# Kernel optimization log

Measured on AMD Instinct MI355X. Metric: run time of the kernel, lower is better.

Reference implementation:

```python
import jax, jax.numpy as jnp
import numpy as np

N, L, V, D, E, NL = 50000, 32, 5000, 128, 800000, 3
P, B = 5000, 64

def setup_inputs() -> dict:
    key = jax.random.key(0)
    ks = jax.random.split(key, 6)
    x = jax.random.randint(ks[0], (N, L), 0, V)            # token ids, 0 = pad
    edge_index = jax.random.randint(ks[1], (2, E), 0, N)   # [2,E] src,dst
    pool_idx = jnp.arange(N) // (N // P)                   # node -> pooled supernode
    node_batch = pool_idx * B // P                         # node -> graph id (grouped, as in torch loop)
    embed = jax.random.normal(ks[2], (V, D), jnp.float32) * 0.02
    W_l = jax.random.normal(ks[3], (NL, D, D), jnp.float32) / np.sqrt(D)
    W_r = jax.random.normal(ks[4], (NL, D, D), jnp.float32) / np.sqrt(D)
    b = jnp.zeros((NL, D), jnp.float32)
    return dict(x=x, edge_index=edge_index, pool_idx=pool_idx, node_batch=node_batch,
                num_pooled=P, embed=embed, W_l=W_l, W_r=W_r, b=b)

def reference(x, edge_index, pool_idx, node_batch, num_pooled, embed, W_l, W_r, b):
    n = x.shape[0]
    dt = embed.dtype
    # masked mean-pool of token embeddings (pad id = 0), length clamped to >=1
    mask = (x != 0)
    lengths = jnp.clip(mask.sum(axis=1), 1, None).astype(dt)          # [N]
    h = (embed[x] * mask[..., None].astype(dt)).sum(axis=1) / lengths[:, None]  # [N,D]
    src, dst = edge_index[0], edge_index[1]
    deg = jnp.clip(jax.ops.segment_sum(jnp.ones(src.shape[0], dt), dst, num_segments=n), 1.0, None)
    # SAGEConv layers: mean-aggregate neighbors, lin_l(agg)+bias + lin_r(self), relu
    # (dropout p=0.5 is identity in eval mode)
    for i in range(W_l.shape[0]):
        agg = jax.ops.segment_sum(h[src], dst, num_segments=n) / deg[:, None]
        h = jax.nn.relu(agg @ W_l[i] + b[i] + h @ W_r[i])
    # global mean pool over supernodes
    cnt = jnp.clip(jax.ops.segment_sum(jnp.ones(n, dt), pool_idx, num_segments=num_pooled), 1.0, None)
    x_pooled = jax.ops.segment_sum(h, pool_idx, num_segments=num_pooled) / cnt[:, None]
    # global max pool of graph ids -> pooled batch vector
    batch_pooled = jax.ops.segment_max(node_batch, pool_idx, num_segments=num_pooled)
    # coalesced pooled edges without self-loops, as a dense boolean adjacency
    sp, dp = pool_idx[src], pool_idx[dst]
    adj = jnp.zeros((num_pooled, num_pooled), jnp.bool_).at[sp, dp].set(True)
    adj = adj & ~jnp.eye(num_pooled, dtype=jnp.bool_)
    return x_pooled, adj, batch_pooled
```

## Files before the change

### kernel.cpp

```cpp
#include <hip/hip_runtime.h>
#include <limits.h>

#define D 128
#define NBK 768
#define EB  2048

typedef __attribute__((ext_vector_type(8))) short bf16x8;
typedef __attribute__((ext_vector_type(4))) float f32x4;

static __device__ __forceinline__ unsigned short f2bf(float f) {
    unsigned u = __builtin_bit_cast(unsigned, f);
    u += 0x7FFFu + ((u >> 16) & 1u);
    return (unsigned short)(u >> 16);
}
static __device__ __forceinline__ float bf2f(unsigned u16) {
    unsigned u = u16 << 16;
    return __builtin_bit_cast(float, u);
}
static __device__ __forceinline__ bf16x8 load_frag(const unsigned short* p) {
    uint4 v = *(const uint4*)p;
    return __builtin_bit_cast(bf16x8, v);
}
static __device__ __forceinline__ void acc8(float* a, uint4 v) {
    a[0] += bf2f(v.x & 0xffff); a[1] += bf2f(v.x >> 16);
    a[2] += bf2f(v.y & 0xffff); a[3] += bf2f(v.y >> 16);
    a[4] += bf2f(v.z & 0xffff); a[5] += bf2f(v.z >> 16);
    a[6] += bf2f(v.w & 0xffff); a[7] += bf2f(v.w >> 16);
}
static __device__ __forceinline__ ushort4 pack4(const float* a, float s) {
    ushort4 o;
    o.x = f2bf(a[0] * s); o.y = f2bf(a[1] * s);
    o.z = f2bf(a[2] * s); o.w = f2bf(a[3] * s);
    return o;
}

__global__ __launch_bounds__(256) void zero_k(float4* __restrict__ b, size_t nb)
{
    size_t i = (size_t)blockIdx.x * 256 + threadIdx.x;
    if (i < nb) b[i] = make_float4(0.f, 0.f, 0.f, 0.f);
}

__global__ __launch_bounds__(256) void epack_k(
    const float* __restrict__ embed, unsigned short* __restrict__ e16, int n4)
{
    int i = blockIdx.x * 256 + threadIdx.x;
    if (i >= n4) return;
    float4 v = *(const float4*)&embed[(size_t)i * 4];
    ushort4 o;
    o.x = f2bf(v.x); o.y = f2bf(v.y); o.z = f2bf(v.z); o.w = f2bf(v.w);
    *(ushort4*)&e16[(size_t)i * 4] = o;
}

__global__ __launch_bounds__(256) void embed_pool_k(
    const int* __restrict__ x, const unsigned short* __restrict__ e16,
    unsigned short* __restrict__ h16, int n, int L)
{
    __shared__ int toks[16][32];
    int t = threadIdx.x;
    int sub = t >> 4, s = t & 15;
    int node = blockIdx.x * 16 + sub;
    for (int j = t; j < 16 * L; j += 256) {
        int nd = blockIdx.x * 16 + j / L;
        toks[j / L][j % L] = (nd < n) ? x[(size_t)nd * L + (j % L)] : 0;
    }
    __syncthreads();
    if (node >= n) return;
    float acc[8] = {};
    int cnt = 0;
    for (int l = 0; l < L; ++l) {
        int tok = toks[sub][l];
        if (tok != 0) {
            acc8(acc, *(const uint4*)&e16[(size_t)tok * D + s * 8]);
            cnt++;
        }
    }
    float inv = 1.0f / (float)(cnt > 0 ? cnt : 1);
    ushort4 lo = pack4(acc, inv), hi = pack4(acc + 4, inv);
    *(ushort4*)&h16[(size_t)node * D + s * 8]     = lo;
    *(ushort4*)&h16[(size_t)node * D + s * 8 + 4] = hi;
}

__global__ __launch_bounds__(256) void wpack_k(
    const float* __restrict__ Wl, const float* __restrict__ Wr,
    unsigned short* __restrict__ Wp, int NL)
{
    int idx = blockIdx.x * 256 + threadIdx.x;
    if (idx >= NL * 2 * 16384) return;
    int m = idx >> 14;
    int r = idx & 16383;
    int j = r & 7;
    int lane = (r >> 3) & 63;
    int cb = (r >> 9) & 7;
    int kb = (r >> 12) & 3;
    const float* W = ((m & 1) ? Wr : Wl) + (size_t)(m >> 1) * D * D;
    int k = kb * 32 + (lane >> 4) * 8 + j;
    int c = cb * 16 + (lane & 15);
    Wp[idx] = f2bf(W[(size_t)k * D + c]);
}

__global__ __launch_bounds__(256) void deghist_k(
    const int* __restrict__ ei, const int* __restrict__ pool,
    int* __restrict__ degall, int E, int n, int P, int nblk)
{
    __shared__ int hist[NBK];
    int t = threadIdx.x;
    for (int i = t; i < NBK; i += 256) hist[i] = 0;
    __syncthreads();
    int base = blockIdx.x * EB;
    int lim = min(E, base + EB);
    for (int e = base + t; e < lim; e += 256) {
        int src = ei[e], dst = ei[E + e];
        atomicAdd(&degall[dst], 1);
        int sp = pool[src], dp = pool[dst];
        if (sp != dp) atomicAdd(&hist[(sp * P + dp) >> 15], 1);
    }
    __syncthreads();
    for (int i = t; i < NBK; i += 256)
        degall[n + i * nblk + blockIdx.x] = hist[i];
}

__global__ __launch_bounds__(256) void scan_partial_k(
    const int* __restrict__ deg, int* __restrict__ bsum, int n)
{
    int b = blockIdx.x, t = threadIdx.x;
    int i0 = b * 1024 + t * 4;
    int s = 0;
    #pragma unroll
    for (int k = 0; k < 4; ++k) { int i = i0 + k; if (i < n) s += deg[i]; }
    for (int off = 32; off > 0; off >>= 1) s += __shfl_down(s, off, 64);
    __shared__ int sm4[4];
    if ((t & 63) == 0) sm4[t >> 6] = s;
    __syncthreads();
    if (t == 0) bsum[b] = sm4[0] + sm4[1] + sm4[2] + sm4[3];
}

__global__ __launch_bounds__(512) void scan_bsum_k(
    const int* __restrict__ bsum, int* __restrict__ boff, int nb)
{
    __shared__ int sm[512];
    int t = threadIdx.x;
    sm[t] = (t < nb) ? bsum[t] : 0;
    __syncthreads();
    for (int off = 1; off < 512; off <<= 1) {
        int add = (t >= off) ? sm[t - off] : 0;
        __syncthreads();
        sm[t] += add;
        __syncthreads();
    }
    if (t < nb) boff[t] = (t > 0) ? sm[t - 1] : 0;
}

__global__ __launch_bounds__(256) void scan_final_k(
    const int* __restrict__ deg, const int* __restrict__ boff,
    int* __restrict__ rp, int n)
{
    __shared__ int sm[256];
    int b = blockIdx.x, t = threadIdx.x;
    int i0 = b * 1024 + t * 4;
    int v[4];
    #pragma unroll
    for (int k = 0; k < 4; ++k) { int i = i0 + k; v[k] = (i < n) ? deg[i] : 0; }
    v[1] += v[0]; v[2] += v[1]; v[3] += v[2];
    sm[t] = v[3];
    __syncthreads();
    for (int off = 1; off < 256; off <<= 1) {
        int add = (t >= off) ? sm[t - off] : 0;
        __syncthreads();
        sm[t] += add;
        __syncthreads();
    }
    int base = boff[b] + ((t > 0) ? sm[t - 1] : 0);
    if (b == 0 && t == 0) rp[0] = 0;
    #pragma unroll
    for (int k = 0; k < 4; ++k) {
        int i = i0 + k;
        if (i < n) rp[i + 1] = base + v[k];
    }
}

__global__ __launch_bounds__(256) void csr_scatter_k(
    const int* __restrict__ ei, const int* __restrict__ rpall,
    int* __restrict__ cur, int* __restrict__ col, int E)
{
    int e = blockIdx.x * 256 + threadIdx.x;
    if (e >= E) return;
    int src = ei[e], dst = ei[E + e];
    int pos = atomicAdd(&cur[dst], 1);
    col[rpall[dst] + pos] = src;
}

__global__ __launch_bounds__(256) void bkt_scatter_k(
    const int* __restrict__ ei, const int* __restrict__ rpall,
    const int* __restrict__ pool, int* __restrict__ kbuf,
    int E, int n, int P, int nblk)
{
    __shared__ int off[NBK];
    int t = threadIdx.x;
    for (int i = t; i < NBK; i += 256)
        off[i] = rpall[n + i * nblk + blockIdx.x] - E;
    __syncthreads();
    int base = blockIdx.x * EB;
    int lim = min(E, base + EB);
    for (int e = base + t; e < lim; e += 256) {
        int src = ei[e], dst = ei[E + e];
        int sp = pool[src], dp = pool[dst];
        if (sp != dp) {
            int key = sp * P + dp;
            int kpos = atomicAdd(&off[key >> 15], 1);
            kbuf[kpos] = key;
        }
    }
}

__global__ __launch_bounds__(256) void adj_write_k(
    const int* __restrict__ rpall, const int* __restrict__ kbuf,
    float* __restrict__ adj, int E, int n, int nblk, int ns)
{
    int b = blockIdx.x;
    int s = rpall[n + b * nblk] - E;
    int e = (b == NBK - 1) ? (rpall[ns] - E) : (rpall[n + (b + 1) * nblk] - E);
    for (int i = s + threadIdx.x; i < e; i += 256)
        adj[(size_t)kbuf[i]] = 1.0f;
}

__global__ __launch_bounds__(256) void aggregate_k(
    const unsigned short* __restrict__ h16, const int* __restrict__ rp,
    const int* __restrict__ col, unsigned short* __restrict__ agg16, int n)
{
    int node = blockIdx.x * 4 + (threadIdx.x >> 6);
    int lane = threadIdx.x & 63;
    if (node >= n) return;
    int beg = rp[node], end = rp[node + 1];
    int q = lane >> 4, s = lane & 15;
    float acc[8] = {};
    int e = beg + q;
    for (; e + 4 < end; e += 8) {
        int s0 = col[e], s1 = col[e + 4];
        uint4 v0 = *(const uint4*)&h16[(size_t)s0 * D + s * 8];
        uint4 v1 = *(const uint4*)&h16[(size_t)s1 * D + s * 8];
        acc8(acc, v0);
        acc8(acc, v1);
    }
    if (e < end)
        acc8(acc, *(const uint4*)&h16[(size_t)col[e] * D + s * 8]);
    #pragma unroll
    for (int k = 0; k < 8; ++k) {
        acc[k] += __shfl_xor(acc[k], 16, 64);
        acc[k] += __shfl_xor(acc[k], 32, 64);
    }
    if (q == 0) {
        int dg = end - beg;
        float inv = 1.0f / (float)(dg > 0 ? dg : 1);
        ushort4 lo = pack4(acc, inv), hi = pack4(acc + 4, inv);
        *(ushort4*)&agg16[(size_t)node * D + s * 8]     = lo;
        *(ushort4*)&agg16[(size_t)node * D + s * 8 + 4] = hi;
    }
}

__global__ __launch_bounds__(256) void sage_gemm_mfma_k(
    const unsigned short* __restrict__ agg16, unsigned short* __restrict__ h16,
    const unsigned short* __restrict__ Wp,
    const float* __restrict__ bias, int n)
{
    int t = threadIdx.x;
    int w = t >> 6, lane = t & 63;
    int node0 = blockIdx.x * 128 + w * 32;
    int row = lane & 15, g = lane >> 4;

    f32x4 acc[2][8];
    #pragma unroll
    for (int i = 0; i < 2; ++i)
        #pragma unroll
        for (int c = 0; c < 8; ++c)
            acc[i][c] = (f32x4){0.f, 0.f, 0.f, 0.f};

    float bs[8];
    #pragma unroll
    for (int cb = 0; cb < 8; ++cb) bs[cb] = bias[cb * 16 + row];

    bool ok0 = (node0 < n);
    bool ok1 = (node0 + 16 < n);

    #pragma unroll
    for (int kb = 0; kb < 8; ++kb) {
        const unsigned short* Asrc = (kb < 4) ? agg16 : h16;
        int ko = (kb & 3) * 32 + g * 8;
        bf16x8 a0 = (bf16x8){0,0,0,0,0,0,0,0};
        bf16x8 a1 = a0;
        if (ok0) a0 = load_frag(&Asrc[(size_t)(node0 + row) * D + ko]);
        if (ok1) a1 = load_frag(&Asrc[(size_t)(node0 + 16 + row) * D + ko]);
        const unsigned short* wp = Wp + ((kb < 4) ? 0 : 16384) + (size_t)(kb & 3) * 4096;
        #pragma unroll
        for (int cb = 0; cb < 8; ++cb) {
            bf16x8 b = load_frag(&wp[(cb * 64 + lane) * 8]);
            acc[0][cb] = __builtin_amdgcn_mfma_f32_16x16x32_bf16(a0, b, acc[0][cb], 0, 0, 0);
            acc[1][cb] = __builtin_amdgcn_mfma_f32_16x16x32_bf16(a1, b, acc[1][cb], 0, 0, 0);
        }
    }

    #pragma unroll
    for (int rg = 0; rg < 2; ++rg) {
        int nb = node0 + rg * 16;
        if (nb >= n) break;
        #pragma unroll
        for (int cb = 0; cb < 8; ++cb) {
            int c = cb * 16 + row;
            #pragma unroll
            for (int j = 0; j < 4; ++j) {
                int node = nb + g * 4 + j;
                float v = fmaxf(acc[rg][cb][j] + bs[cb], 0.f);
                h16[(size_t)node * D + c] = f2bf(v);
            }
        }
    }
}

__global__ __launch_bounds__(128) void poolmean_k(
    const unsigned short* __restrict__ h16, const int* __restrict__ pool,
    const int* __restrict__ nbatch, float* __restrict__ outx,
    float* __restrict__ outb, int n, int P)
{
    int p = blockIdx.x;
    int d = threadIdx.x;
    int lo = 0, hi = n;
    while (lo < hi) { int mid = (lo + hi) >> 1; if (pool[mid] < p) lo = mid + 1; else hi = mid; }
    int s = lo;
    hi = n;
    while (lo < hi) { int mid = (lo + hi) >> 1; if (pool[mid] < p + 1) lo = mid + 1; else hi = mid; }
    int e = lo;
    float sum = 0.f;
    for (int i = s; i < e; ++i) sum += bf2f(h16[(size_t)i * D + d]);
    int c = e - s;
    outx[(size_t)p * D + d] = sum / (float)(c > 0 ? c : 1);
    if (d == 0) {
        int bm = INT_MIN;
        for (int i = s; i < e; ++i) bm = max(bm, nbatch[i]);
        outb[p] = (float)bm;
    }
}

extern "C" void kernel_launch(void* const* d_in, const int* in_sizes, int n_in,
                              void* d_out, int out_size, void* d_ws, size_t ws_size,
                              hipStream_t stream)
{
    const int*   x      = (const int*)d_in[0];
    const int*   ei     = (const int*)d_in[1];
    const int*   pool   = (const int*)d_in[2];
    const int*   nbatch = (const int*)d_in[3];
    const float* embed  = (const float*)d_in[5];
    const float* Wl     = (const float*)d_in[6];
    const float* Wr     = (const float*)d_in[7];
    const float* bias   = (const float*)d_in[8];

    const int N  = in_sizes[2];
    const int L  = in_sizes[0] / N;
    const int E  = in_sizes[1] / 2;
    const int VD = in_sizes[5];
    const int NL = in_sizes[6] / (D * D);
    const int P  = 5000;

    float* out_x   = (float*)d_out;
    float* out_adj = out_x + (size_t)P * D;
    float* out_b   = out_adj + (size_t)P * P;

    char* w = (char*)d_ws;
    auto alloc = [&](size_t bytes) { void* p = w; w += (bytes + 255) & ~255ULL; return p; };
    size_t ND = (size_t)N * D;
    unsigned short* h16   = (unsigned short*)alloc(ND * 2);
    unsigned short* agg16 = (unsigned short*)alloc(ND * 2);
    unsigned short* Wp    = (unsigned short*)alloc((size_t)NL * 2 * 16384 * 2);
    unsigned short* e16   = (unsigned short*)alloc((size_t)VD * 2);

    const int NBLK = (E + EB - 1) / EB;
    const int NS   = N + NBK * NBLK;
    const int NB   = (NS + 1023) / 1024;

    int*   col    = (int*)alloc((size_t)E * 4);
    int*   kbuf   = (int*)alloc((size_t)E * 4);
    int*   rpall  = (int*)alloc((size_t)(NS + 1) * 4);
    int*   bsum   = (int*)alloc(512 * 4);
    int*   boff   = (int*)alloc(512 * 4);
    int*   degall = (int*)alloc((size_t)(NS + N) * 4);
    int*   cur    = degall + NS;

    size_t nz = ((size_t)(NS + N) + 3) / 4;
    zero_k<<<(int)((nz + 255) / 256), 256, 0, stream>>>((float4*)degall, nz);

    epack_k<<<(VD / 4 + 255) / 256, 256, 0, stream>>>(embed, e16, VD / 4);
    wpack_k<<<(NL * 2 * 16384 + 255) / 256, 256, 0, stream>>>(Wl, Wr, Wp, NL);
    embed_pool_k<<<(N + 15) / 16, 256, 0, stream>>>(x, e16, h16, N, L);
    deghist_k<<<NBLK, 256, 0, stream>>>(ei, pool, degall, E, N, P, NBLK);
    scan_partial_k<<<NB, 256, 0, stream>>>(degall, bsum, NS);
    scan_bsum_k<<<1, 512, 0, stream>>>(bsum, boff, NB);
    scan_final_k<<<NB, 256, 0, stream>>>(degall, boff, rpall, NS);
    csr_scatter_k<<<(E + 255) / 256, 256, 0, stream>>>(ei, rpall, cur, col, E);
    bkt_scatter_k<<<NBLK, 256, 0, stream>>>(ei, rpall, pool, kbuf, E, N, P, NBLK);
    adj_write_k<<<NBK, 256, 0, stream>>>(rpall, kbuf, out_adj, E, N, NBLK, NS);

    for (int ly = 0; ly < NL; ++ly) {
        aggregate_k<<<(N + 3) / 4, 256, 0, stream>>>(h16, rpall, col, agg16, N);
        sage_gemm_mfma_k<<<(N + 127) / 128, 256, 0, stream>>>(
            agg16, h16, Wp + (size_t)ly * 2 * 16384, bias + (size_t)ly * D, N);
    }

    poolmean_k<<<P, 128, 0, stream>>>(h16, pool, nbatch, out_x, out_b, N, P);
}
```

Baseline: 308.4 us.

## Store node features and embeddings in scaled FP8 for neighbor aggregation gathers

Adds a scaled FP8 copy of the node feature matrix, written by the embedding pool and GEMM kernels, and has the neighbor aggregation gather from it instead of the bf16 copy. This halves the bytes per random gather. The embedding table is also stored as FP8 and gathered in that form. Aggregation lanes now cover 16 features each, so 8 edges are processed in parallel per wave. The cost is reduced precision in both the aggregated messages and the initial features, plus extra byte-wise stores in the GEMM epilogue.

```diff
diff --git a/kernel.cpp b/kernel.cpp
--- a/kernel.cpp
+++ b/kernel.cpp
@@ -1,12 +1,19 @@
 #include <hip/hip_runtime.h>
+#include <hip/hip_fp16.h>
 #include <limits.h>
 
 #define D 128
 #define NBK 768
 #define EB  2048
+#define SCL 64.0f
 
 typedef __attribute__((ext_vector_type(8))) short bf16x8;
 typedef __attribute__((ext_vector_type(4))) float f32x4;
+typedef __attribute__((ext_vector_type(2))) float f32x2;
+
+#if __has_builtin(__builtin_amdgcn_cvt_pk_f32_fp8) && __has_builtin(__builtin_amdgcn_cvt_pk_fp8_f32)
+#define HW_FP8 1
+#endif
 
 static __device__ __forceinline__ unsigned short f2bf(float f) {
     unsigned u = __builtin_bit_cast(unsigned, f);
@@ -20,12 +27,6 @@
 static __device__ __forceinline__ bf16x8 load_frag(const unsigned short* p) {
     uint4 v = *(const uint4*)p;
     return __builtin_bit_cast(bf16x8, v);
-}
-static __device__ __forceinline__ void acc8(float* a, uint4 v) {
-    a[0] += bf2f(v.x & 0xffff); a[1] += bf2f(v.x >> 16);
-    a[2] += bf2f(v.y & 0xffff); a[3] += bf2f(v.y >> 16);
-    a[4] += bf2f(v.z & 0xffff); a[5] += bf2f(v.z >> 16);
-    a[6] += bf2f(v.w & 0xffff); a[7] += bf2f(v.w >> 16);
 }
 static __device__ __forceinline__ ushort4 pack4(const float* a, float s) {
     ushort4 o;
@@ -34,6 +35,41 @@
     return o;
 }
 
+static __device__ __forceinline__ unsigned char f2q(float v) {
+#ifdef HW_FP8
+    return (unsigned char)(__builtin_amdgcn_cvt_pk_fp8_f32(v, v, 0, false) & 0xff);
+#else
+    unsigned short u = __half_as_ushort(__float2half(v));
+    u = (unsigned short)(u + 0x7F + ((u >> 8) & 1));
+    return (unsigned char)(u >> 8);
+#endif
+}
+static __device__ __forceinline__ unsigned enc4(float a0, float a1, float a2, float a3) {
+#ifdef HW_FP8
+    unsigned u = __builtin_amdgcn_cvt_pk_fp8_f32(a0, a1, 0, false);
+    u = __builtin_amdgcn_cvt_pk_fp8_f32(a2, a3, (int)u, true);
+    return u;
+#else
+    return (unsigned)f2q(a0) | ((unsigned)f2q(a1) << 8) |
+           ((unsigned)f2q(a2) << 16) | ((unsigned)f2q(a3) << 24);
+#endif
+}
+static __device__ __forceinline__ void dec4(float* a, unsigned u) {
+#ifdef HW_FP8
+    f32x2 lo = __builtin_amdgcn_cvt_pk_f32_fp8((int)u, false);
+    f32x2 hi = __builtin_amdgcn_cvt_pk_f32_fp8((int)u, true);
+    a[0] += lo.x; a[1] += lo.y; a[2] += hi.x; a[3] += hi.y;
+#else
+    a[0] += __half2float(__ushort_as_half((unsigned short)((u & 0xff) << 8)));
+    a[1] += __half2float(__ushort_as_half((unsigned short)(((u >> 8) & 0xff) << 8)));
+    a[2] += __half2float(__ushort_as_half((unsigned short)(((u >> 16) & 0xff) << 8)));
+    a[3] += __half2float(__ushort_as_half((unsigned short)((u >> 24) << 8)));
+#endif
+}
+static __device__ __forceinline__ void dec16(float* a, uint4 v) {
+    dec4(a, v.x); dec4(a + 4, v.y); dec4(a + 8, v.z); dec4(a + 12, v.w);
+}
+
 __global__ __launch_bounds__(256) void zero_k(float4* __restrict__ b, size_t nb)
 {
     size_t i = (size_t)blockIdx.x * 256 + threadIdx.x;
@@ -41,19 +77,17 @@
 }
 
 __global__ __launch_bounds__(256) void epack_k(
-    const float* __restrict__ embed, unsigned short* __restrict__ e16, int n4)
+    const float* __restrict__ embed, unsigned* __restrict__ e8, int n4)
 {
     int i = blockIdx.x * 256 + threadIdx.x;
     if (i >= n4) return;
     float4 v = *(const float4*)&embed[(size_t)i * 4];
-    ushort4 o;
-    o.x = f2bf(v.x); o.y = f2bf(v.y); o.z = f2bf(v.z); o.w = f2bf(v.w);
-    *(ushort4*)&e16[(size_t)i * 4] = o;
+    e8[i] = enc4(v.x * SCL, v.y * SCL, v.z * SCL, v.w * SCL);
 }
 
 __global__ __launch_bounds__(256) void embed_pool_k(
-    const int* __restrict__ x, const unsigned short* __restrict__ e16,
-    unsigned short* __restrict__ h16, int n, int L)
+    const int* __restrict__ x, const unsigned char* __restrict__ e8,
+    unsigned short* __restrict__ h16, unsigned char* __restrict__ h8, int n, int L)
 {
     __shared__ int toks[16][32];
     int t = threadIdx.x;
@@ -70,14 +104,21 @@
     for (int l = 0; l < L; ++l) {
         int tok = toks[sub][l];
         if (tok != 0) {
-            acc8(acc, *(const uint4*)&e16[(size_t)tok * D + s * 8]);
+            uint2 v = *(const uint2*)&e8[(size_t)tok * D + s * 8];
+            dec4(acc, v.x); dec4(acc + 4, v.y);
             cnt++;
         }
     }
-    float inv = 1.0f / (float)(cnt > 0 ? cnt : 1);
-    ushort4 lo = pack4(acc, inv), hi = pack4(acc + 4, inv);
+    float c = (float)(cnt > 0 ? cnt : 1);
+    float invh = 1.0f / (SCL * c);
+    float inv8 = 1.0f / c;
+    ushort4 lo = pack4(acc, invh), hi = pack4(acc + 4, invh);
     *(ushort4*)&h16[(size_t)node * D + s * 8]     = lo;
     *(ushort4*)&h16[(size_t)node * D + s * 8 + 4] = hi;
+    uint2 q;
+    q.x = enc4(acc[0] * inv8, acc[1] * inv8, acc[2] * inv8, acc[3] * inv8);
+    q.y = enc4(acc[4] * inv8, acc[5] * inv8, acc[6] * inv8, acc[7] * inv8);
+    *(uint2*)&h8[(size_t)node * D + s * 8] = q;
 }
 
 __global__ __launch_bounds__(256) void wpack_k(
@@ -224,43 +265,46 @@
 }
 
 __global__ __launch_bounds__(256) void aggregate_k(
-    const unsigned short* __restrict__ h16, const int* __restrict__ rp,
+    const unsigned char* __restrict__ h8, const int* __restrict__ rp,
     const int* __restrict__ col, unsigned short* __restrict__ agg16, int n)
 {
     int node = blockIdx.x * 4 + (threadIdx.x >> 6);
     int lane = threadIdx.x & 63;
     if (node >= n) return;
     int beg = rp[node], end = rp[node + 1];
-    int q = lane >> 4, s = lane & 15;
-    float acc[8] = {};
-    int e = beg + q;
-    for (; e + 4 < end; e += 8) {
-        int s0 = col[e], s1 = col[e + 4];
-        uint4 v0 = *(const uint4*)&h16[(size_t)s0 * D + s * 8];
-        uint4 v1 = *(const uint4*)&h16[(size_t)s1 * D + s * 8];
-        acc8(acc, v0);
-        acc8(acc, v1);
+    int oct = lane >> 3, s = lane & 7;
+    float acc[16] = {};
+    int e = beg + oct;
+    for (; e + 8 < end; e += 16) {
+        uint4 v0 = *(const uint4*)&h8[(size_t)col[e] * D + s * 16];
+        uint4 v1 = *(const uint4*)&h8[(size_t)col[e + 8] * D + s * 16];
+        dec16(acc, v0);
+        dec16(acc, v1);
     }
     if (e < end)
-        acc8(acc, *(const uint4*)&h16[(size_t)col[e] * D + s * 8]);
-    #pragma unroll
-    for (int k = 0; k < 8; ++k) {
+        dec16(acc, *(const uint4*)&h8[(size_t)col[e] * D + s * 16]);
+    #pragma unroll
+    for (int k = 0; k < 16; ++k) {
+        acc[k] += __shfl_xor(acc[k], 8, 64);
         acc[k] += __shfl_xor(acc[k], 16, 64);
         acc[k] += __shfl_xor(acc[k], 32, 64);
     }
-    if (q == 0) {
+    if (oct == 0) {
         int dg = end - beg;
-        float inv = 1.0f / (float)(dg > 0 ? dg : 1);
-        ushort4 lo = pack4(acc, inv), hi = pack4(acc + 4, inv);
-        *(ushort4*)&agg16[(size_t)node * D + s * 8]     = lo;
-        *(ushort4*)&agg16[(size_t)node * D + s * 8 + 4] = hi;
+        float inv = 1.0f / (SCL * (float)(dg > 0 ? dg : 1));
+        ushort4 o0 = pack4(acc, inv),     o1 = pack4(acc + 4, inv);
+        ushort4 o2 = pack4(acc + 8, inv), o3 = pack4(acc + 12, inv);
+        *(ushort4*)&agg16[(size_t)node * D + s * 16]      = o0;
+        *(ushort4*)&agg16[(size_t)node * D + s * 16 + 4]  = o1;
+        *(ushort4*)&agg16[(size_t)node * D + s * 16 + 8]  = o2;
+        *(ushort4*)&agg16[(size_t)node * D + s * 16 + 12] = o3;
     }
 }
 
 __global__ __launch_bounds__(256) void sage_gemm_mfma_k(
     const unsigned short* __restrict__ agg16, unsigned short* __restrict__ h16,
-    const unsigned short* __restrict__ Wp,
-    const float* __restrict__ bias, int n)
+    unsigned char* __restrict__ h8, const unsigned short* __restrict__ Wp,
+    const float* __restrict__ bias, int n, int write8)
 {
     int t = threadIdx.x;
     int w = t >> 6, lane = t & 63;
@@ -310,6 +354,7 @@
                 int node = nb + g * 4 + j;
                 float v = fmaxf(acc[rg][cb][j] + bs[cb], 0.f);
                 h16[(size_t)node * D + c] = f2bf(v);
+                if (write8) h8[(size_t)node * D + c] = f2q(v * SCL);
             }
         }
     }
@@ -368,8 +413,9 @@
     size_t ND = (size_t)N * D;
     unsigned short* h16   = (unsigned short*)alloc(ND * 2);
     unsigned short* agg16 = (unsigned short*)alloc(ND * 2);
+    unsigned char*  h8    = (unsigned char*)alloc(ND);
     unsigned short* Wp    = (unsigned short*)alloc((size_t)NL * 2 * 16384 * 2);
-    unsigned short* e16   = (unsigned short*)alloc((size_t)VD * 2);
+    unsigned char*  e8    = (unsigned char*)alloc((size_t)VD);
 
     const int NBLK = (E + EB - 1) / EB;
     const int NS   = N + NBK * NBLK;
@@ -386,9 +432,9 @@
     size_t nz = ((size_t)(NS + N) + 3) / 4;
     zero_k<<<(int)((nz + 255) / 256), 256, 0, stream>>>((float4*)degall, nz);
 
-    epack_k<<<(VD / 4 + 255) / 256, 256, 0, stream>>>(embed, e16, VD / 4);
+    epack_k<<<(VD / 4 + 255) / 256, 256, 0, stream>>>(embed, (unsigned*)e8, VD / 4);
     wpack_k<<<(NL * 2 * 16384 + 255) / 256, 256, 0, stream>>>(Wl, Wr, Wp, NL);
-    embed_pool_k<<<(N + 15) / 16, 256, 0, stream>>>(x, e16, h16, N, L);
+    embed_pool_k<<<(N + 15) / 16, 256, 0, stream>>>(x, e8, h16, h8, N, L);
     deghist_k<<<NBLK, 256, 0, stream>>>(ei, pool, degall, E, N, P, NBLK);
     scan_partial_k<<<NB, 256, 0, stream>>>(degall, bsum, NS);
     scan_bsum_k<<<1, 512, 0, stream>>>(bsum, boff, NB);
@@ -398,9 +444,10 @@
     adj_write_k<<<NBK, 256, 0, stream>>>(rpall, kbuf, out_adj, E, N, NBLK, NS);
 
     for (int ly = 0; ly < NL; ++ly) {
-        aggregate_k<<<(N + 3) / 4, 256, 0, stream>>>(h16, rpall, col, agg16, N);
+        aggregate_k<<<(N + 3) / 4, 256, 0, stream>>>(h8, rpall, col, agg16, N);
         sage_gemm_mfma_k<<<(N + 127) / 128, 256, 0, stream>>>(
-            agg16, h16, Wp + (size_t)ly * 2 * 16384, bias + (size_t)ly * D, N);
+            agg16, h16, h8, Wp + (size_t)ly * 2 * 16384, bias + (size_t)ly * D, N,
+            (ly < NL - 1) ? 1 : 0);
     }
 
     poolmean_k<<<P, 128, 0, stream>>>(h16, pool, nbatch, out_x, out_b, N, P);
```

Measured after the change: 308.9 us. No clear change (+0.2%).
